# Performance work log

Hardware: AMD Instinct MI355X
Metric: run time of the kernel (lower is better)

## Reference

```python
import jax, jax.numpy as jnp
import numpy as np

D_MODEL, N_HEAD, D_HEAD = 192, 16, 6
INNER = N_HEAD * D_HEAD  # 96
LN_EPS = 1e-9
INF = 1e6


def _rel_pos_embeds(S):
    # Funnel get_position_embeds, relative_shift path, block 0
    half = D_MODEL // 2
    freq = jnp.arange(half, dtype=jnp.float32)
    inv_freq = 1.0 / (10000.0 ** (freq / half))
    rel_pos_id = jnp.arange(-2 * S, 2 * S, dtype=jnp.float32)  # [4S]
    sinusoid = rel_pos_id[:, None] * inv_freq[None, :]          # [4S, half]
    pos_embed = jnp.concatenate([jnp.sin(sinusoid), jnp.cos(sinusoid)], axis=-1)  # [4S, D]
    # block 0: relative_pos(pos, stride=1) = arange(S, -S, -1), offset by 2S
    idx = jnp.arange(S, -S, -1) + 2 * S  # [2S]
    return pos_embed[idx]  # [2S, D]


def _relative_shift_gather(pos_attn, context_len):
    # shift = 1 (q_len == context_len)
    B, n, S, M = pos_attn.shape  # M = 2*S
    pa = pos_attn.reshape(B, n, M, S)[:, :, 1:, :]
    pa = pa.reshape(B, n, S, M - 1)[..., :context_len]
    return pa


def setup_inputs() -> dict:
    key = jax.random.key(0)
    ks = jax.random.split(key, 12)
    B, S = 4, 1024
    s = 0.02
    return {
        "x": jax.random.normal(ks[0], (B, S, D_MODEL), dtype=jnp.float32),
        "mask0": jnp.ones((B, S), dtype=jnp.float32),
        "Wq": jax.random.normal(ks[1], (D_MODEL, INNER), dtype=jnp.float32) * s,
        "Wk": jax.random.normal(ks[2], (D_MODEL, INNER), dtype=jnp.float32) * s,
        "bk": jnp.zeros((INNER,), dtype=jnp.float32),
        "Wv": jax.random.normal(ks[3], (D_MODEL, INNER), dtype=jnp.float32) * s,
        "bv": jnp.zeros((INNER,), dtype=jnp.float32),
        "Wo": jax.random.normal(ks[4], (INNER, D_MODEL), dtype=jnp.float32) * s,
        "bo": jnp.zeros((D_MODEL,), dtype=jnp.float32),
        "r_w_bias": jax.random.normal(ks[5], (N_HEAD, D_HEAD), dtype=jnp.float32) * s,
        "r_r_bias": jax.random.normal(ks[6], (N_HEAD, D_HEAD), dtype=jnp.float32) * s,
        "r_kernel": jax.random.normal(ks[7], (D_MODEL, N_HEAD, D_HEAD), dtype=jnp.float32) * s,
        "gamma": jnp.ones((D_MODEL,), dtype=jnp.float32),
        "beta": jnp.zeros((D_MODEL,), dtype=jnp.float32),
    }


def reference(x, mask0, Wq, Wk, bk, Wv, bv, Wo, bo, r_w_bias, r_r_bias, r_kernel, gamma, beta):
    B, S, _ = x.shape
    scale = 1.0 / np.sqrt(D_HEAD).astype(np.float32)

    q = (x @ Wq).reshape(B, S, N_HEAD, D_HEAD) * scale       # q_head pre-scaled
    k = (x @ Wk + bk).reshape(B, S, N_HEAD, D_HEAD)
    v = (x @ Wv + bv).reshape(B, S, N_HEAD, D_HEAD)

    # content score
    content = jnp.einsum("bind,bjnd->bnij", q + r_w_bias * scale, k)

    # positional score with relative shift
    r = _rel_pos_embeds(S)                                    # [2S, D]
    r_head = jnp.einsum("td,dnh->tnh", r, r_kernel)           # [2S, n, h]
    pos_attn = jnp.einsum("binh,tnh->bnit", q + r_r_bias * scale, r_head)  # [B,n,S,2S]
    pos_attn = _relative_shift_gather(pos_attn, S)            # [B,n,S,S]

    attn_score = content + pos_attn  # token_type_attn = 0 (no token_type_ids)
    attn_score = attn_score - INF * (1.0 - mask0[:, None, None, :])
    attn_prob = jax.nn.softmax(attn_score, axis=-1)

    attn_vec = jnp.einsum("bnij,bjnd->bind", attn_prob, v)    # [B,S,n,h]
    attn_out = attn_vec.reshape(B, S, INNER) @ Wo + bo

    h = x + attn_out
    mu = jnp.mean(h, axis=-1, keepdims=True)
    var = jnp.mean(jnp.square(h - mu), axis=-1, keepdims=True)
    out = (h - mu) / jnp.sqrt(var + LN_EPS) * gamma + beta
    return out
```

## Files before the change

### kernel.cpp

```cpp
#include <hip/hip_runtime.h>
#include <hip/hip_bf16.h>
#include <math.h>

#define LOG2E 1.4426950408889634f
#define IS6   0.4082482904638630f

typedef _Float16 h2 __attribute__((ext_vector_type(2)));

#if defined(__has_builtin)
#if __has_builtin(__builtin_amdgcn_fdot2)
#define FDOT2(a,b,c) __builtin_amdgcn_fdot2((a),(b),(c),false)
#endif
#endif
#ifndef FDOT2
#define FDOT2(a,b,c) ((float)(a).x*(float)(b).x + (float)(a).y*(float)(b).y + (c))
#endif

__device__ __forceinline__ unsigned packh2(float x, float y) {
    h2 v; v.x = (_Float16)x; v.y = (_Float16)y;
    return *(unsigned*)&v;
}
__device__ __forceinline__ h2 ash2(unsigned u) { return *(h2*)&u; }
__device__ __forceinline__ unsigned ah2(h2 v) { return *(unsigned*)&v; }

__device__ __forceinline__ float fdot2_asm(h2 a, h2 b, float c) {
    float d;
    asm("v_dot2_f32_f16 %0, %1, %2, %3" : "=v"(d) : "v"(a), "v"(b), "v"(c));
    return d;
}
__device__ __forceinline__ float exp2_asm(float x) {
    float r;
    asm("v_exp_f32 %0, %1" : "=v"(r) : "v"(x));
    return r;
}

#if defined(__has_builtin)
#if __has_builtin(__builtin_amdgcn_cvt_pkrtz)
__device__ __forceinline__ h2 pk2(float a, float b) {
    auto r = __builtin_amdgcn_cvt_pkrtz(a, b);
    union { decltype(r) f; h2 h; } c; c.f = r; return c.h;
}
#define HAVE_PK2 1
#endif
#endif
#ifndef HAVE_PK2
__device__ __forceinline__ h2 pk2(float a, float b) {
    h2 v; v.x = (_Float16)a; v.y = (_Float16)b; return v;
}
#endif

__global__ __launch_bounds__(96)
void k_wpack(const float* __restrict__ Wq, const float* __restrict__ Wk,
             const float* __restrict__ Wv, uint4* __restrict__ Whp4) {
    int cq = blockIdx.x;
    int dp = threadIdx.x;
    int mat = cq / 24, c0 = (cq - mat * 24) * 4;
    const float* W = mat == 0 ? Wq : (mat == 1 ? Wk : Wv);
    float4 r0 = *(const float4*)&W[(2 * dp) * 96 + c0];
    float4 r1 = *(const float4*)&W[(2 * dp + 1) * 96 + c0];
    uint4 v;
    v.x = packh2(r0.x, r1.x);
    v.y = packh2(r0.y, r1.y);
    v.z = packh2(r0.z, r1.z);
    v.w = packh2(r0.w, r1.w);
    Whp4[cq * 96 + dp] = v;
}

__global__ __launch_bounds__(256)
void k_pre(const float* __restrict__ x, const uint4* __restrict__ Whp4,
           const float* __restrict__ bk, const float* __restrict__ bv,
           const float* __restrict__ rwb, const float* __restrict__ rrb,
           const float* __restrict__ rk,
           unsigned* __restrict__ QWt, unsigned* __restrict__ QRt,
           unsigned* __restrict__ Kpl, unsigned* __restrict__ Vpl,
           unsigned short* __restrict__ phiB) {
    __shared__ unsigned xs[64 * 97];
    __shared__ float rrowS[4 * 192];
    int tid = threadIdx.x;
    if (blockIdx.x < 1152) {
        int rt = blockIdx.x / 18, qb = blockIdx.x - rt * 18;
        int row0 = rt * 64;
        for (int idx = tid; idx < 6144; idx += 256) {
            int r = idx / 96, dpp = idx - r * 96;
            float2 xv = *(const float2*)&x[(size_t)(row0 + r) * 192 + dpp * 2];
            xs[r * 97 + dpp] = packh2(xv.x, xv.y);
        }
        __syncthreads();
        int quad = __builtin_amdgcn_readfirstlane(tid >> 6);
        int sl = tid & 63;
        int cq = qb * 4 + quad;
        int c0g = cq * 4;
        int mat = c0g / 96, col0 = c0g - mat * 96;
        const uint4* wb = Whp4 + cq * 96;
        const unsigned* xr = xs + sl * 97;
        float a0 = 0.f, a1 = 0.f, a2 = 0.f, a3 = 0.f;
        #pragma unroll 8
        for (int dp = 0; dp < 96; ++dp) {
            uint4 w4 = wb[dp];
            h2 xp = ash2(xr[dp]);
            a0 = FDOT2(xp, ash2(w4.x), a0);
            a1 = FDOT2(xp, ash2(w4.y), a1);
            a2 = FDOT2(xp, ash2(w4.z), a2);
            a3 = FDOT2(xp, ash2(w4.w), a3);
        }
        float av[4] = {a0, a1, a2, a3};
        int row = row0 + sl, b = row >> 10, s = row & 1023;
        if (mat == 0) {
            #pragma unroll
            for (int pp = 0; pp < 2; ++pp) {
                int cA = col0 + 2 * pp;
                int pg = cA >> 1;
                int nn = pg / 3, hp = pg - nn * 3;
                int bnn = b * 16 + nn;
                unsigned qw = packh2((av[2*pp]   + rwb[cA])   * (IS6 * LOG2E),
                                     (av[2*pp+1] + rwb[cA+1]) * (IS6 * LOG2E));
                unsigned qr = packh2((av[2*pp]   + rrb[cA])   * (IS6 * LOG2E),
                                     (av[2*pp+1] + rrb[cA+1]) * (IS6 * LOG2E));
                size_t qo = ((size_t)(hp * 64 + bnn) << 10) + s;
                QWt[qo] = qw;
                QRt[qo] = qr;
            }
        } else if (mat == 1) {
            #pragma unroll
            for (int pp = 0; pp < 2; ++pp) {
                int cA = col0 + 2 * pp;
                int pg = cA >> 1;
                int nn = pg / 3, hp = pg - nn * 3;
                int bnn = b * 16 + nn;
                Kpl[((size_t)(hp * 64 + bnn) << 10) + s] =
                    packh2(av[2*pp] + bk[cA], av[2*pp+1] + bk[cA+1]);
            }
        } else {
            #pragma unroll
            for (int pp = 0; pp < 2; ++pp) {
                int cA = col0 + 2 * pp;
                int pg = cA >> 1;
                int nn = pg / 3, hp = pg - nn * 3;
                int bnn = b * 16 + nn;
                Vpl[((size_t)(hp * 64 + bnn) << 10) + s] =
                    packh2(av[2*pp] + bv[cA], av[2*pp+1] + bv[cA+1]);
            }
        }
    } else {
        int t0 = (blockIdx.x - 1152) * 4;
        for (int idx = tid; idx < 768; idx += 256) {
            int tl = idx / 192, d = idx - tl * 192;
            int dd = d < 96 ? d : d - 96;
            float w = exp2f(-(float)dd * 0.13841367062030676f);
            float ang = (float)(1024 - (t0 + tl)) * w;
            rrowS[idx] = (d < 96) ? __sinf(ang) : __cosf(ang);
        }
        __syncthreads();
        if (tid < 192) {
            int c = tid % 96, tg = tid / 96;
            float acc0 = 0.f, acc1 = 0.f;
            #pragma unroll 4
            for (int d = 0; d < 192; ++d) {
                float wv = rk[d * 96 + c];
                acc0 += rrowS[(tg * 2 + 0) * 192 + d] * wv;
                acc1 += rrowS[(tg * 2 + 1) * 192 + d] * wv;
            }
            int n = c / 6, h = c - n * 6;
            _Float16 v0 = (_Float16)acc0, v1 = (_Float16)acc1;
            phiB[(n * 2048 + t0 + tg * 2 + 0) * 8 + h] = *(unsigned short*)&v0;
            phiB[(n * 2048 + t0 + tg * 2 + 1) * 8 + h] = *(unsigned short*)&v1;
            if (tg == 0 && c < 32) {
                int nn = c >> 1, hh = 6 + (c & 1);
                #pragma unroll
                for (int k = 0; k < 4; ++k)
                    phiB[(nn * 2048 + t0 + k) * 8 + hh] = 0;
            }
        }
    }
}

#define SWZ(r) ((r) ^ (((r) >> 2) & 7))
__global__ __launch_bounds__(256, 4)
void k_attn(const unsigned* __restrict__ QWt, const unsigned* __restrict__ QRt,
            const unsigned* __restrict__ Kpl, const unsigned* __restrict__ Vpl,
            const float* __restrict__ mask0,
            const unsigned short* __restrict__ phiB,
            uint4* __restrict__ P) {
    __shared__ uint4 phiS[1056];
    __shared__ uint4 kS[33];
    __shared__ uint4 vS[33];
    int tid = threadIdx.x;
    int jc = blockIdx.x, n = blockIdx.y, b = blockIdx.z;
    int j0 = jc * 32;
    int bn = b * 16 + n;

    const uint4* phg = (const uint4*)phiB + (n * 2048 + j0 + 1);
    for (int r = tid; r < 1056; r += 256) phiS[SWZ(r)] = phg[r];
    if (tid < 32) {
        int j = j0 + tid;
        size_t base = ((size_t)bn << 10) + j;
        float mt = 1e6f * (mask0[b * 1024 + j] - 1.0f) * LOG2E;
        kS[tid] = make_uint4(Kpl[base], Kpl[base + 65536], Kpl[base + 131072],
                             __float_as_uint(mt));
    } else if (tid < 64) {
        int r = tid - 32;
        int j = j0 + r;
        size_t base = ((size_t)bn << 10) + j;
        vS[r] = make_uint4(Vpl[base], Vpl[base + 65536], Vpl[base + 131072], 0u);
    } else if (tid == 64) {
        kS[32] = make_uint4(0u, 0u, 0u, 0u);
        vS[32] = make_uint4(0u, 0u, 0u, 0u);
    }
    __syncthreads();

    int iA = tid * 4;
    h2 qw[4][3], qr[4][3];
    #pragma unroll
    for (int hp = 0; hp < 3; ++hp) {
        size_t off = (size_t)hp * 65536 + ((size_t)bn << 10) + iA;
        uint4 qa = *(const uint4*)&QWt[off];
        qw[0][hp] = ash2(qa.x); qw[1][hp] = ash2(qa.y);
        qw[2][hp] = ash2(qa.z); qw[3][hp] = ash2(qa.w);
        uint4 ra = *(const uint4*)&QRt[off];
        qr[0][hp] = ash2(ra.x); qr[1][hp] = ash2(ra.y);
        qr[2][hp] = ash2(ra.z); qr[3][hp] = ash2(ra.w);
    }

    float den[4] = {0.f, 0.f, 0.f, 0.f};
    h2 zero2; zero2.x = (_Float16)0.f; zero2.y = (_Float16)0.f;
    h2 ac0[4], ac1[4], ac2[4];
    #pragma unroll
    for (int q = 0; q < 4; ++q) { ac0[q] = zero2; ac1[q] = zero2; ac2[q] = zero2; }

    int Cb = 1023 - iA;
    uint4 ph[4];
    ph[3] = phiS[SWZ(Cb - 1)];
    ph[2] = phiS[SWZ(Cb - 2)];
    ph[1] = phiS[SWZ(Cb - 3)];
    uint4 nxt = phiS[SWZ(Cb)];
    uint4 Kc = kS[0], Vc = vS[0];

    #pragma unroll 4
    for (int jj = 0; jj < 32; ++jj) {
        uint4 K = Kc, V = Vc;
        ph[jj & 3] = nxt;
        Kc = kS[jj + 1];
        Vc = vS[jj + 1];
        nxt = phiS[SWZ(Cb + jj + 1)];
        float mt = __uint_as_float(K.w);
        h2 v01 = ash2(V.x), v23 = ash2(V.y), v45 = ash2(V.z);
        #pragma unroll
        for (int q = 0; q < 4; ++q) {
            uint4 p = ph[(jj - q) & 3];
            float sc = fdot2_asm(ash2(K.x), qw[q][0],
                       fdot2_asm(ash2(K.y), qw[q][1],
                       fdot2_asm(ash2(K.z), qw[q][2], mt)));
            sc = fdot2_asm(ash2(p.x), qr[q][0],
                 fdot2_asm(ash2(p.y), qr[q][1],
                 fdot2_asm(ash2(p.z), qr[q][2], sc)));
            float e = exp2_asm(sc);
            den[q] += e;
            h2 e2 = pk2(e, e);
            ac0[q] += e2 * v01;
            ac1[q] += e2 * v23;
            ac2[q] += e2 * v45;
        }
    }
    size_t pb = ((size_t)(jc * 64 + bn)) << 10;
    #pragma unroll
    for (int q = 0; q < 4; ++q) {
        uint4 st;
        st.x = __float_as_uint(den[q]);
        st.y = ah2(ac0[q]); st.z = ah2(ac1[q]); st.w = ah2(ac2[q]);
        P[pb + q * 256 + tid] = st;
    }
}

__global__ __launch_bounds__(256)
void k_comb(const uint4* __restrict__ P, float* __restrict__ AV) {
    int flat = blockIdx.x * 256 + threadIdx.x;
    int bn = flat >> 10, rem = flat & 1023;
    int q = rem >> 8, tt = rem & 255;
    int i = tt * 4 + q;
    int b = bn >> 4, n = bn & 15;
    float d = 0.f, s0 = 0.f, s1 = 0.f, s2 = 0.f, s3 = 0.f, s4 = 0.f, s5 = 0.f;
    #pragma unroll 8
    for (int jc = 0; jc < 32; ++jc) {
        uint4 u = P[(((size_t)(jc * 64 + bn)) << 10) + rem];
        h2 x0 = ash2(u.y), x1 = ash2(u.z), x2 = ash2(u.w);
        d  += __uint_as_float(u.x);
        s0 += (float)x0.x; s1 += (float)x0.y;
        s2 += (float)x1.x; s3 += (float)x1.y;
        s4 += (float)x2.x; s5 += (float)x2.y;
    }
    float inv = 1.0f / d;
    float* o = AV + ((size_t)(b * 1024 + i)) * 96 + n * 6;
    o[0] = s0 * inv; o[1] = s1 * inv; o[2] = s2 * inv;
    o[3] = s3 * inv; o[4] = s4 * inv; o[5] = s5 * inv;
}

__global__ __launch_bounds__(256)
void k_out(const float* __restrict__ AV, const float* __restrict__ Wo,
           const float* __restrict__ bo, const float* __restrict__ x,
           const float* __restrict__ gamma, const float* __restrict__ beta,
           float* __restrict__ out) {
    __shared__ unsigned WoS[96 * 96];
    __shared__ float avS[8 * 96];
    int tid = threadIdx.x;
    int row0 = blockIdx.x * 8;
    for (int idx = tid; idx < 9216; idx += 256) {
        int c = idx / 96, pd = idx - c * 96;
        float2 w = *(const float2*)&Wo[c * 192 + pd * 2];
        WoS[idx] = packh2(w.x, w.y);
    }
    for (int idx = tid; idx < 768; idx += 256)
        avS[idx] = AV[(size_t)row0 * 96 + idx];
    __syncthreads();

    int lane = tid & 63, wv = tid >> 6;
    bool act = lane < 48;
    int d0 = lane * 4;
    #pragma unroll
    for (int rr = 0; rr < 2; ++rr) {
        int r = wv * 2 + rr, row = row0 + r;
        float ax = 0.f, ay = 0.f, az = 0.f, aw = 0.f;
        if (act) {
            float4 bq = *(const float4*)&bo[d0];
            float4 xq = *(const float4*)&x[(size_t)row * 192 + d0];
            ax = bq.x + xq.x; ay = bq.y + xq.y; az = bq.z + xq.z; aw = bq.w + xq.w;
            for (int c2 = 0; c2 < 96; ++c2) {
                float a = avS[r * 96 + c2];
                uint2 wp = *(uint2*)&WoS[c2 * 96 + lane * 2];
                h2 w0 = ash2(wp.x), w1 = ash2(wp.y);
                ax += a * (float)w0.x; ay += a * (float)w0.y;
                az += a * (float)w1.x; aw += a * (float)w1.y;
            }
        }
        float sum = act ? (ax + ay + az + aw) : 0.f;
        #pragma unroll
        for (int off = 32; off; off >>= 1) sum += __shfl_xor(sum, off, 64);
        float mu = sum * (1.0f / 192.0f);
        float dx = ax - mu, dy = ay - mu, dz = az - mu, dw = aw - mu;
        float vs = act ? (dx * dx + dy * dy + dz * dz + dw * dw) : 0.f;
        #pragma unroll
        for (int off = 32; off; off >>= 1) vs += __shfl_xor(vs, off, 64);
        float rstd = rsqrtf(vs * (1.0f / 192.0f) + 1e-9f);
        if (act) {
            float4 g = *(const float4*)&gamma[d0];
            float4 bb = *(const float4*)&beta[d0];
            float4 rv;
            rv.x = dx * rstd * g.x + bb.x;
            rv.y = dy * rstd * g.y + bb.y;
            rv.z = dz * rstd * g.z + bb.z;
            rv.w = dw * rstd * g.w + bb.w;
            *(float4*)&out[(size_t)row * 192 + d0] = rv;
        }
    }
}

extern "C" void kernel_launch(void* const* d_in, const int* in_sizes, int n_in,
                              void* d_out, int out_size, void* d_ws, size_t ws_size,
                              hipStream_t stream) {
    const float* x        = (const float*)d_in[0];
    const float* mask0    = (const float*)d_in[1];
    const float* Wq       = (const float*)d_in[2];
    const float* Wk       = (const float*)d_in[3];
    const float* bk       = (const float*)d_in[4];
    const float* Wv       = (const float*)d_in[5];
    const float* bv       = (const float*)d_in[6];
    const float* Wo       = (const float*)d_in[7];
    const float* bo       = (const float*)d_in[8];
    const float* rwb      = (const float*)d_in[9];
    const float* rrb      = (const float*)d_in[10];
    const float* r_kernel = (const float*)d_in[11];
    const float* gamma    = (const float*)d_in[12];
    const float* beta     = (const float*)d_in[13];
    float* out = (float*)d_out;

    unsigned* QWt = (unsigned*)d_ws;
    unsigned* QRt = QWt + 196608;
    unsigned* Kpl = QRt + 196608;
    unsigned* Vpl = Kpl + 196608;
    uint4*    P   = (uint4*)(Vpl + 196608);
    unsigned short* phiB = (unsigned short*)(P + 2097152);
    uint4*    Whp4 = (uint4*)(phiB + 262144);
    float*    AV  = (float*)(Whp4 + 6912);

    k_wpack<<<72, 96, 0, stream>>>(Wq, Wk, Wv, Whp4);
    k_pre<<<1664, 256, 0, stream>>>(x, Whp4, bk, bv, rwb, rrb, r_kernel,
                                    QWt, QRt, Kpl, Vpl, phiB);
    k_attn<<<dim3(32, 16, 4), 256, 0, stream>>>(QWt, QRt, Kpl, Vpl, mask0, phiB, P);
    k_comb<<<256, 256, 0, stream>>>(P, AV);
    k_out<<<512, 256, 0, stream>>>(AV, Wo, bo, x, gamma, beta, out);
}
```

Before: 92.94 us.

## Fuse weight packing and split-K combine into neighbours, double attention key chunk

Weight fp16 packing moves into k_pre, where each block packs its own slice into LDS, and the positional-projection blocks are now scheduled first. k_attn processes 64 keys per block instead of 32, which halves the number of partial results. The split-K reduction (k_comb) is folded into k_out so partials are reduced directly into shared memory. Together these remove two launches and the AV round trip through global memory. The cost is lower attention grid parallelism and redundant weight packing in every QKV block.

```diff
diff --git a/kernel.cpp b/kernel.cpp
--- a/kernel.cpp
+++ b/kernel.cpp
@@ -49,25 +49,10 @@
 }
 #endif
 
-__global__ __launch_bounds__(96)
-void k_wpack(const float* __restrict__ Wq, const float* __restrict__ Wk,
-             const float* __restrict__ Wv, uint4* __restrict__ Whp4) {
-    int cq = blockIdx.x;
-    int dp = threadIdx.x;
-    int mat = cq / 24, c0 = (cq - mat * 24) * 4;
-    const float* W = mat == 0 ? Wq : (mat == 1 ? Wk : Wv);
-    float4 r0 = *(const float4*)&W[(2 * dp) * 96 + c0];
-    float4 r1 = *(const float4*)&W[(2 * dp + 1) * 96 + c0];
-    uint4 v;
-    v.x = packh2(r0.x, r1.x);
-    v.y = packh2(r0.y, r1.y);
-    v.z = packh2(r0.z, r1.z);
-    v.w = packh2(r0.w, r1.w);
-    Whp4[cq * 96 + dp] = v;
-}
-
 __global__ __launch_bounds__(256)
-void k_pre(const float* __restrict__ x, const uint4* __restrict__ Whp4,
+void k_pre(const float* __restrict__ x,
+           const float* __restrict__ Wq, const float* __restrict__ Wk,
+           const float* __restrict__ Wv,
            const float* __restrict__ bk, const float* __restrict__ bv,
            const float* __restrict__ rwb, const float* __restrict__ rrb,
            const float* __restrict__ rk,
@@ -75,15 +60,61 @@
            unsigned* __restrict__ Kpl, unsigned* __restrict__ Vpl,
            unsigned short* __restrict__ phiB) {
     __shared__ unsigned xs[64 * 97];
+    __shared__ uint4 Wlds[384];
     __shared__ float rrowS[4 * 192];
     int tid = threadIdx.x;
-    if (blockIdx.x < 1152) {
-        int rt = blockIdx.x / 18, qb = blockIdx.x - rt * 18;
+    if (blockIdx.x < 512) {
+        int t0 = blockIdx.x * 4;
+        for (int idx = tid; idx < 768; idx += 256) {
+            int tl = idx / 192, d = idx - tl * 192;
+            int dd = d < 96 ? d : d - 96;
+            float w = exp2f(-(float)dd * 0.13841367062030676f);
+            float ang = (float)(1024 - (t0 + tl)) * w;
+            rrowS[idx] = (d < 96) ? __sinf(ang) : __cosf(ang);
+        }
+        __syncthreads();
+        if (tid < 192) {
+            int c = tid % 96, tg = tid / 96;
+            float acc0 = 0.f, acc1 = 0.f;
+            #pragma unroll 4
+            for (int d = 0; d < 192; ++d) {
+                float wv = rk[d * 96 + c];
+                acc0 += rrowS[(tg * 2 + 0) * 192 + d] * wv;
+                acc1 += rrowS[(tg * 2 + 1) * 192 + d] * wv;
+            }
+            int n = c / 6, h = c - n * 6;
+            _Float16 v0 = (_Float16)acc0, v1 = (_Float16)acc1;
+            phiB[(n * 2048 + t0 + tg * 2 + 0) * 8 + h] = *(unsigned short*)&v0;
+            phiB[(n * 2048 + t0 + tg * 2 + 1) * 8 + h] = *(unsigned short*)&v1;
+            if (tg == 0 && c < 32) {
+                int nn = c >> 1, hh = 6 + (c & 1);
+                #pragma unroll
+                for (int k = 0; k < 4; ++k)
+                    phiB[(nn * 2048 + t0 + k) * 8 + hh] = 0;
+            }
+        }
+    } else {
+        int qkvb = blockIdx.x - 512;
+        int rt = qkvb / 18, qb = qkvb - rt * 18;
         int row0 = rt * 64;
         for (int idx = tid; idx < 6144; idx += 256) {
             int r = idx / 96, dpp = idx - r * 96;
             float2 xv = *(const float2*)&x[(size_t)(row0 + r) * 192 + dpp * 2];
             xs[r * 97 + dpp] = packh2(xv.x, xv.y);
+        }
+        for (int idx = tid; idx < 384; idx += 256) {
+            int quad = idx / 96, dp = idx - quad * 96;
+            int cq = qb * 4 + quad;
+            int mat = cq / 24, c0 = (cq - mat * 24) * 4;
+            const float* W = mat == 0 ? Wq : (mat == 1 ? Wk : Wv);
+            float4 r0 = *(const float4*)&W[(2 * dp) * 96 + c0];
+            float4 r1 = *(const float4*)&W[(2 * dp + 1) * 96 + c0];
+            uint4 v;
+            v.x = packh2(r0.x, r1.x);
+            v.y = packh2(r0.y, r1.y);
+            v.z = packh2(r0.z, r1.z);
+            v.w = packh2(r0.w, r1.w);
+            Wlds[idx] = v;
         }
         __syncthreads();
         int quad = __builtin_amdgcn_readfirstlane(tid >> 6);
@@ -91,7 +122,7 @@
         int cq = qb * 4 + quad;
         int c0g = cq * 4;
         int mat = c0g / 96, col0 = c0g - mat * 96;
-        const uint4* wb = Whp4 + cq * 96;
+        const uint4* wb = &Wlds[quad * 96];
         const unsigned* xr = xs + sl * 97;
         float a0 = 0.f, a1 = 0.f, a2 = 0.f, a3 = 0.f;
         #pragma unroll 8
@@ -141,36 +172,6 @@
                     packh2(av[2*pp] + bv[cA], av[2*pp+1] + bv[cA+1]);
             }
         }
-    } else {
-        int t0 = (blockIdx.x - 1152) * 4;
-        for (int idx = tid; idx < 768; idx += 256) {
-            int tl = idx / 192, d = idx - tl * 192;
-            int dd = d < 96 ? d : d - 96;
-            float w = exp2f(-(float)dd * 0.13841367062030676f);
-            float ang = (float)(1024 - (t0 + tl)) * w;
-            rrowS[idx] = (d < 96) ? __sinf(ang) : __cosf(ang);
-        }
-        __syncthreads();
-        if (tid < 192) {
-            int c = tid % 96, tg = tid / 96;
-            float acc0 = 0.f, acc1 = 0.f;
-            #pragma unroll 4
-            for (int d = 0; d < 192; ++d) {
-                float wv = rk[d * 96 + c];
-                acc0 += rrowS[(tg * 2 + 0) * 192 + d] * wv;
-                acc1 += rrowS[(tg * 2 + 1) * 192 + d] * wv;
-            }
-            int n = c / 6, h = c - n * 6;
-            _Float16 v0 = (_Float16)acc0, v1 = (_Float16)acc1;
-            phiB[(n * 2048 + t0 + tg * 2 + 0) * 8 + h] = *(unsigned short*)&v0;
-            phiB[(n * 2048 + t0 + tg * 2 + 1) * 8 + h] = *(unsigned short*)&v1;
-            if (tg == 0 && c < 32) {
-                int nn = c >> 1, hh = 6 + (c & 1);
-                #pragma unroll
-                for (int k = 0; k < 4; ++k)
-                    phiB[(nn * 2048 + t0 + k) * 8 + hh] = 0;
-            }
-        }
     }
 }
 
@@ -181,30 +182,30 @@
             const float* __restrict__ mask0,
             const unsigned short* __restrict__ phiB,
             uint4* __restrict__ P) {
-    __shared__ uint4 phiS[1056];
-    __shared__ uint4 kS[33];
-    __shared__ uint4 vS[33];
+    __shared__ uint4 phiS[1088];
+    __shared__ uint4 kS[65];
+    __shared__ uint4 vS[65];
     int tid = threadIdx.x;
     int jc = blockIdx.x, n = blockIdx.y, b = blockIdx.z;
-    int j0 = jc * 32;
+    int j0 = jc * 64;
     int bn = b * 16 + n;
 
     const uint4* phg = (const uint4*)phiB + (n * 2048 + j0 + 1);
-    for (int r = tid; r < 1056; r += 256) phiS[SWZ(r)] = phg[r];
-    if (tid < 32) {
+    for (int r = tid; r < 1088; r += 256) phiS[SWZ(r)] = phg[r];
+    if (tid < 64) {
         int j = j0 + tid;
         size_t base = ((size_t)bn << 10) + j;
         float mt = 1e6f * (mask0[b * 1024 + j] - 1.0f) * LOG2E;
         kS[tid] = make_uint4(Kpl[base], Kpl[base + 65536], Kpl[base + 131072],
                              __float_as_uint(mt));
-    } else if (tid < 64) {
-        int r = tid - 32;
+    } else if (tid < 128) {
+        int r = tid - 64;
         int j = j0 + r;
         size_t base = ((size_t)bn << 10) + j;
         vS[r] = make_uint4(Vpl[base], Vpl[base + 65536], Vpl[base + 131072], 0u);
-    } else if (tid == 64) {
-        kS[32] = make_uint4(0u, 0u, 0u, 0u);
-        vS[32] = make_uint4(0u, 0u, 0u, 0u);
+    } else if (tid == 128) {
+        kS[64] = make_uint4(0u, 0u, 0u, 0u);
+        vS[64] = make_uint4(0u, 0u, 0u, 0u);
     }
     __syncthreads();
 
@@ -236,7 +237,7 @@
     uint4 Kc = kS[0], Vc = vS[0];
 
     #pragma unroll 4
-    for (int jj = 0; jj < 32; ++jj) {
+    for (int jj = 0; jj < 64; ++jj) {
         uint4 K = Kc, V = Vc;
         ph[jj & 3] = nxt;
         Kc = kS[jj + 1];
@@ -272,30 +273,7 @@
 }
 
 __global__ __launch_bounds__(256)
-void k_comb(const uint4* __restrict__ P, float* __restrict__ AV) {
-    int flat = blockIdx.x * 256 + threadIdx.x;
-    int bn = flat >> 10, rem = flat & 1023;
-    int q = rem >> 8, tt = rem & 255;
-    int i = tt * 4 + q;
-    int b = bn >> 4, n = bn & 15;
-    float d = 0.f, s0 = 0.f, s1 = 0.f, s2 = 0.f, s3 = 0.f, s4 = 0.f, s5 = 0.f;
-    #pragma unroll 8
-    for (int jc = 0; jc < 32; ++jc) {
-        uint4 u = P[(((size_t)(jc * 64 + bn)) << 10) + rem];
-        h2 x0 = ash2(u.y), x1 = ash2(u.z), x2 = ash2(u.w);
-        d  += __uint_as_float(u.x);
-        s0 += (float)x0.x; s1 += (float)x0.y;
-        s2 += (float)x1.x; s3 += (float)x1.y;
-        s4 += (float)x2.x; s5 += (float)x2.y;
-    }
-    float inv = 1.0f / d;
-    float* o = AV + ((size_t)(b * 1024 + i)) * 96 + n * 6;
-    o[0] = s0 * inv; o[1] = s1 * inv; o[2] = s2 * inv;
-    o[3] = s3 * inv; o[4] = s4 * inv; o[5] = s5 * inv;
-}
-
-__global__ __launch_bounds__(256)
-void k_out(const float* __restrict__ AV, const float* __restrict__ Wo,
+void k_out(const uint4* __restrict__ P, const float* __restrict__ Wo,
            const float* __restrict__ bo, const float* __restrict__ x,
            const float* __restrict__ gamma, const float* __restrict__ beta,
            float* __restrict__ out) {
@@ -308,8 +286,26 @@
         float2 w = *(const float2*)&Wo[c * 192 + pd * 2];
         WoS[idx] = packh2(w.x, w.y);
     }
-    for (int idx = tid; idx < 768; idx += 256)
-        avS[idx] = AV[(size_t)row0 * 96 + idx];
+    if (tid < 128) {
+        int n = tid >> 3, rl = tid & 7;
+        int row = row0 + rl, b = row >> 10, i = row & 1023;
+        int bn = b * 16 + n;
+        int q = i & 3, tt = i >> 2;
+        float d = 0.f, s0 = 0.f, s1 = 0.f, s2 = 0.f, s3 = 0.f, s4 = 0.f, s5 = 0.f;
+        #pragma unroll
+        for (int jc = 0; jc < 16; ++jc) {
+            uint4 u = P[(((size_t)(jc * 64 + bn)) << 10) + q * 256 + tt];
+            h2 x0 = ash2(u.y), x1 = ash2(u.z), x2 = ash2(u.w);
+            d  += __uint_as_float(u.x);
+            s0 += (float)x0.x; s1 += (float)x0.y;
+            s2 += (float)x1.x; s3 += (float)x1.y;
+            s4 += (float)x2.x; s5 += (float)x2.y;
+        }
+        float inv = 1.0f / d;
+        float* o = &avS[rl * 96 + n * 6];
+        o[0] = s0 * inv; o[1] = s1 * inv; o[2] = s2 * inv;
+        o[3] = s3 * inv; o[4] = s4 * inv; o[5] = s5 * inv;
+    }
     __syncthreads();
 
     int lane = tid & 63, wv = tid >> 6;
@@ -377,14 +373,10 @@
     unsigned* Kpl = QRt + 196608;
     unsigned* Vpl = Kpl + 196608;
     uint4*    P   = (uint4*)(Vpl + 196608);
-    unsigned short* phiB = (unsigned short*)(P + 2097152);
-    uint4*    Whp4 = (uint4*)(phiB + 262144);
-    float*    AV  = (float*)(Whp4 + 6912);
-
-    k_wpack<<<72, 96, 0, stream>>>(Wq, Wk, Wv, Whp4);
-    k_pre<<<1664, 256, 0, stream>>>(x, Whp4, bk, bv, rwb, rrb, r_kernel,
+    unsigned short* phiB = (unsigned short*)(P + 1048576);
+
+    k_pre<<<1664, 256, 0, stream>>>(x, Wq, Wk, Wv, bk, bv, rwb, rrb, r_kernel,
                                     QWt, QRt, Kpl, Vpl, phiB);
-    k_attn<<<dim3(32, 16, 4), 256, 0, stream>>>(QWt, QRt, Kpl, Vpl, mask0, phiB, P);
-    k_comb<<<256, 256, 0, stream>>>(P, AV);
-    k_out<<<512, 256, 0, stream>>>(AV, Wo, bo, x, gamma, beta, out);
-}
+    k_attn<<<dim3(16, 16, 4), 256, 0, stream>>>(QWt, QRt, Kpl, Vpl, mask0, phiB, P);
+    k_out<<<512, 256, 0, stream>>>(P, Wo, bo, x, gamma, beta, out);
+}
```

Measured after the change: 94.69 us. No clear change (+1.9%).
